# Kernel optimization log

Measured on AMD Instinct MI355X. Metric: run time of the kernel, lower is better.

## Reference

```python
import jax, jax.numpy as jnp
import numpy as np
import math

HIDDEN = 1024
HEADS = 16
HEAD = HIDDEN // HEADS
B, N = 2, 2048
NEG_INF = -10000.0


def setup_inputs() -> dict:
    key = jax.random.key(0)
    k1, k2, k3, k4, k5 = jax.random.split(key, 5)
    s = 1.0 / math.sqrt(HIDDEN)
    return {
        "encodings": jax.random.normal(k1, (B, N, HIDDEN), dtype=jnp.float32),
        "attn_w": jax.random.uniform(k2, (3 * HIDDEN, HIDDEN), minval=-s, maxval=s, dtype=jnp.float32),
        "attn_b": jax.random.uniform(k3, (3 * HIDDEN,), minval=-s, maxval=s, dtype=jnp.float32),
        "out_w": jax.random.uniform(k4, (HIDDEN, HIDDEN), minval=-s, maxval=s, dtype=jnp.float32),
        "out_b": jax.random.uniform(k5, (HIDDEN,), minval=-s, maxval=s, dtype=jnp.float32),
    }


def reference(encodings, attn_w, attn_b, out_w, out_b):
    b, n, _ = encodings.shape
    qkv = encodings @ attn_w.T + attn_b                      # [b, n, 3*hidden]
    # 'b n (h l) -> b h n l' with l = 3*head_size
    qkv = qkv.reshape(b, n, HEADS, 3 * HEAD).transpose(0, 2, 1, 3)  # [b, h, n, 3d]
    q, k, v = jnp.split(qkv, 3, axis=-1)                     # each [b, h, n, d]
    # causal mask: key index k attends only if k <= q
    mask = jnp.arange(n)[:, None] <= jnp.arange(n)[None, :]  # [k, q]
    scores = jnp.einsum('bhki,bhqi->bhkq', k, q) / math.sqrt(HEAD)
    scores = jnp.where(mask, scores, NEG_INF)
    probs = jax.nn.softmax(scores, axis=2)                   # softmax over k
    combined = jnp.einsum('bhkq,bhkl->bhql', probs, v)       # [b, h, n, d]
    out = combined.transpose(0, 2, 1, 3).reshape(b, n, HIDDEN)
    return out @ out_w.T + out_b
```

## Files before the change

kernel.cpp:

```cpp
#include <hip/hip_runtime.h>
#include <hip/hip_bf16.h>
#include <stdint.h>

#define HIDDEN 1024
#define NHEADS 16
#define DHEAD  64
#define BATCH  2
#define SEQ    2048
#define MROWS  (BATCH*SEQ)
#define QKVC   (3*HIDDEN)

typedef unsigned short u16;
typedef unsigned int   u32;
typedef __bf16 bf16x8 __attribute__((ext_vector_type(8)));
typedef __bf16 bf16x2 __attribute__((ext_vector_type(2)));
typedef float  f32x4  __attribute__((ext_vector_type(4)));
typedef float  f32x16 __attribute__((ext_vector_type(16)));
typedef short  s16x4  __attribute__((ext_vector_type(4)));
typedef u16    u16x8  __attribute__((ext_vector_type(8)));
typedef u32    u32x2  __attribute__((ext_vector_type(2)));

typedef const __attribute__((address_space(1))) void gvoid_t;
typedef       __attribute__((address_space(3))) void lvoid_t;

__device__ __forceinline__ gvoid_t* to_glob(const void* p){
  return (gvoid_t*)(uintptr_t)p;
}
__device__ __forceinline__ lvoid_t* to_lds(void* p){
  return (lvoid_t*)(uintptr_t)p;
}
__device__ __forceinline__ u32 lds_off(const void* p){
  return (u32)(uintptr_t)p;
}

__device__ __forceinline__ u16 f2bf(float x){
  __bf16 h = (__bf16)x;
  return __builtin_bit_cast(u16, h);
}
__device__ __forceinline__ u32 pk2(float a, float b){
  bf16x2 t = { (__bf16)a, (__bf16)b };
  return __builtin_bit_cast(u32, t);
}

#define MFMA32(a, b, c) __builtin_amdgcn_mfma_f32_32x32x16_bf16(a, b, c, 0, 0, 0)

#define CVT_N0 1048576
#define CVT_N1  786432
#define CVT_N2  262144
__global__ __launch_bounds__(256) void k_cvt3(const float* __restrict__ e,
                                              const float* __restrict__ wa,
                                              const float* __restrict__ wo,
                                              u16* __restrict__ eb,
                                              u16* __restrict__ wab,
                                              u16* __restrict__ wob){
  int i = blockIdx.x * 256 + threadIdx.x;
  const float* src; u16* dst;
  if (i < CVT_N0){ src = e; dst = eb; }
  else if (i < CVT_N0 + CVT_N1){ i -= CVT_N0; src = wa; dst = wab; }
  else if (i < CVT_N0 + CVT_N1 + CVT_N2){ i -= CVT_N0 + CVT_N1; src = wo; dst = wob; }
  else return;
  const float4 v = reinterpret_cast<const float4*>(src)[i];
  ushort4 o;
  o.x = f2bf(v.x); o.y = f2bf(v.y); o.z = f2bf(v.z); o.w = f2bf(v.w);
  reinterpret_cast<ushort4*>(dst)[i] = o;
}

template<int NC, bool BF16OUT>
__global__ __launch_bounds__(256) void k_gemm(const u16* __restrict__ A,
                                              const u16* __restrict__ B,
                                              const float* __restrict__ bias,
                                              void* __restrict__ C){
  constexpr int K = HIDDEN;
  __shared__ u16 As[2][128*32];
  __shared__ u16 Bs[2][128*32];
  const int lin = blockIdx.x + gridDim.x * blockIdx.y;
  const int xcd = lin & 7;
  const int pos = lin >> 3;
  const int mt  = pos & 31;
  const int nt  = xcd * (gridDim.y >> 3) + (pos >> 5);
  const int m0 = mt * 128;
  const int n0 = nt * 128;
  const int tid = threadIdx.x;
  const int w = tid >> 6, l = tid & 63;
  const int wr = w >> 1, wc = w & 1;

  const f32x4 fz = {0.f, 0.f, 0.f, 0.f};
  f32x4 acc[4][4];
  #pragma unroll
  for (int i = 0; i < 4; ++i)
    #pragma unroll
    for (int j = 0; j < 4; ++j) acc[i][j] = fz;

  const u16* ap = A + (size_t)(m0 + (tid >> 2)) * K + (tid & 3) * 8;
  const u16* bp = B + (size_t)(n0 + (tid >> 2)) * K + (tid & 3) * 8;

  auto stage = [&](int k0, int buf){
    __builtin_amdgcn_global_load_lds(to_glob(ap + k0),        to_lds(&As[buf][w*512]),        16, 0, 0);
    __builtin_amdgcn_global_load_lds(to_glob(ap + 64*K + k0), to_lds(&As[buf][2048 + w*512]), 16, 0, 0);
    __builtin_amdgcn_global_load_lds(to_glob(bp + k0),        to_lds(&Bs[buf][w*512]),        16, 0, 0);
    __builtin_amdgcn_global_load_lds(to_glob(bp + 64*K + k0), to_lds(&Bs[buf][2048 + w*512]), 16, 0, 0);
  };

  stage(0, 0);
  __syncthreads();

  for (int k0 = 0; k0 < K; k0 += 32){
    const int cur = (k0 >> 5) & 1;
    if (k0 + 32 < K) stage(k0 + 32, cur ^ 1);

    bf16x8 af[4], bfr[4];
    #pragma unroll
    for (int mf = 0; mf < 4; ++mf)
      af[mf]  = *(const bf16x8*)&As[cur][(wr*64 + mf*16 + (l & 15))*32 + (l >> 4)*8];
    #pragma unroll
    for (int nf = 0; nf < 4; ++nf)
      bfr[nf] = *(const bf16x8*)&Bs[cur][(wc*64 + nf*16 + (l & 15))*32 + (l >> 4)*8];
    #pragma unroll
    for (int mf = 0; mf < 4; ++mf)
      #pragma unroll
      for (int nf = 0; nf < 4; ++nf)
        acc[mf][nf] = __builtin_amdgcn_mfma_f32_16x16x32_bf16(af[mf], bfr[nf], acc[mf][nf], 0, 0, 0);

    __syncthreads();
  }

  #pragma unroll
  for (int nf = 0; nf < 4; ++nf){
    const int col = n0 + wc*64 + nf*16 + (l & 15);
    const float bv = bias[col];
    #pragma unroll
    for (int mf = 0; mf < 4; ++mf){
      #pragma unroll
      for (int r = 0; r < 4; ++r){
        const int row = m0 + wr*64 + mf*16 + (l >> 4)*4 + r;
        const float v = acc[mf][nf][r] + bv;
        if constexpr (BF16OUT) ((u16*)C)[(size_t)row * NC + col] = f2bf(v);
        else                   ((float*)C)[(size_t)row * NC + col] = v;
      }
    }
  }
}

__global__ __launch_bounds__(256, 4) void k_attn(const u16* __restrict__ qkv,
                                                 u16* __restrict__ aout){
  __shared__ u16 smem[20480];

  const int bh = blockIdx.x;
  const int b  = bh >> 4;
  const int h  = bh & 15;
  const int qt = 31 - blockIdx.y;
  const int tid = threadIdx.x;
  const int l  = tid & 63;
  const int w  = tid >> 6;
  const int hr = w >> 1;
  const int wr = w & 1;
  const int t128 = tid & 127;
  const int lw = t128 >> 6;
  const int U  = qt + 1;
  const int kb = hr ? U : 0;
  const int kmax = kb + U - 1;
  const int q0 = qt*64 + wr*32;
  const size_t base = (size_t)b * SEQ * QKVC + (size_t)h * 192;
  const float CEXP = 0.18033688011112042f;

  u16* const Kreg = smem + hr*10240;
  u16* const Vreg = smem + hr*10240 + 6144;

  const int cgK = (t128 & 7) ^ ((t128 >> 3) & 7);
  const u16* const baseK = qkv + base + (size_t)(t128 >> 3) * QKVC + 64 + cgK * 8;
  const int vk = ((t128 >> 5) << 2) | ((t128 >> 1) & 3);
  const int vd = (((t128 >> 3) & 3) << 4) | ((t128 & 1) << 3);
  const u16* const baseV = qkv + base + (size_t)vk * QKVC + 128 + vd;

  auto stageK = [&](int u, int cb){
    const u16* pk = baseK + (size_t)u * 32 * QKVC;
    #pragma unroll
    for (int t = 0; t < 2; ++t)
      __builtin_amdgcn_global_load_lds(to_glob(pk + t*16*QKVC),
                                       to_lds(&Kreg[cb*2048 + t*1024 + lw*512]), 16, 0, 0);
  };
  auto stageV = [&](int u, int vb){
    const u16* pv = baseV + (size_t)u * 32 * QKVC;
    #pragma unroll
    for (int t = 0; t < 2; ++t)
      __builtin_amdgcn_global_load_lds(to_glob(pv + t*16*QKVC),
                                       to_lds(&Vreg[vb*2048 + t*1024 + lw*512]), 16, 0, 0);
  };

  bf16x8 qf[4];
  {
    const u16* qp = qkv + base + (size_t)(q0 + (l & 31)) * QKVC + (l >> 5) * 8;
    #pragma unroll
    for (int dd = 0; dd < 4; ++dd) qf[dd] = *(const bf16x8*)(qp + dd*16);
  }

  f32x16 o0{}, o1{};
  float m = -1e30f, lsum = 0.f;

  stageK(kb, 0);
  stageV(kb, 0);
  stageK(kb + (U > 1 ? 1 : 0), 1);

  const u32 vbytes = lds_off(Vreg) + (l & 15)*8 + ((l >> 4) & 1)*128 + (l >> 5)*1024;

  int cb3 = 0;
  int vb2 = 0;
  for (int it = 0; it < U; ++it){
    const int u = kb + it;

    asm volatile("s_waitcnt vmcnt(2)" ::: "memory");
    __builtin_amdgcn_sched_barrier(0);
    __builtin_amdgcn_s_barrier();
    __builtin_amdgcn_sched_barrier(0);

    stageV(u + 1 > kmax ? kmax : u + 1, vb2 ^ 1);
    stageK(u + 2 > kmax ? kmax : u + 2, cb3 == 0 ? 2 : cb3 - 1);

    f32x16 a0{};
    const int r0 = l & 31;
    __builtin_amdgcn_s_setprio(1);
    #pragma unroll
    for (int dd = 0; dd < 4; ++dd){
      const int c = dd*2 + (l >> 5);
      const bf16x8 k0 = *(const bf16x8*)&Kreg[cb3*2048 + r0*64 + ((c ^ (r0 & 7)))*8];
      a0 = MFMA32(k0, qf[dd], a0);
    }
    __builtin_amdgcn_s_setprio(0);

    if (u*32 + 31 > q0){
      const int qg = q0 + (l & 31);
      #pragma unroll
      for (int r = 0; r < 16; ++r){
        const int kg = u*32 + (r & 3) + 8*(r >> 2) + 4*(l >> 5);
        if (kg > qg) a0[r] = -1e30f;
      }
    }

    float t8[8];
    #pragma unroll
    for (int r = 0; r < 8; ++r) t8[r] = fmaxf(a0[2*r], a0[2*r + 1]);
    #pragma unroll
    for (int s = 4; s > 0; s >>= 1)
      #pragma unroll
      for (int r = 0; r < s; ++r) t8[r] = fmaxf(t8[r], t8[r + s]);
    float pm = t8[0];
    pm = fmaxf(pm, __shfl(pm, l ^ 32));

    s16x4 tr[8];
    {
      const u32 vb = vbytes + (u32)vb2 * 4096u;
      #pragma unroll
      for (int kk = 0; kk < 2; ++kk){
        asm volatile("ds_read_b64_tr_b16 %0, %4 offset:0\n\t"
                     "ds_read_b64_tr_b16 %1, %4 offset:512\n\t"
                     "ds_read_b64_tr_b16 %2, %4 offset:256\n\t"
                     "ds_read_b64_tr_b16 %3, %4 offset:768"
                     : "=&v"(tr[kk*4+0]), "=&v"(tr[kk*4+1]),
                       "=&v"(tr[kk*4+2]), "=&v"(tr[kk*4+3])
                     : "v"(vb + kk*2048));
      }
    }

    if (__any(pm > m + 64.f)){
      const float mn = fmaxf(m, pm);
      const float corr = exp2f((m - mn) * CEXP);
      m = mn;
      lsum *= corr;
      #pragma unroll
      for (int r = 0; r < 16; ++r){
        const int row = (r & 3) + 8*(r >> 2) + 4*(l >> 5);
        const float cr = __shfl(corr, row | (l & 32));
        o0[r] *= cr; o1[r] *= cr;
      }
    }
    {
      float ls0 = 0.f, ls1 = 0.f;
      #pragma unroll
      for (int r = 0; r < 16; r += 2){
        const float p0 = exp2f((a0[r]   - m) * CEXP);
        const float p1 = exp2f((a0[r+1] - m) * CEXP);
        ls0 += p0; ls1 += p1;
        a0[r] = p0; a0[r+1] = p1;
      }
      lsum += ls0 + ls1;
    }

    asm volatile("s_waitcnt lgkmcnt(0)" ::: "memory");
    __builtin_amdgcn_sched_barrier(0);
    __builtin_amdgcn_s_setprio(1);
    #pragma unroll
    for (int kk = 0; kk < 2; ++kk){
      const int o = kk * 8;
      const u32 x0 = pk2(a0[o+0], a0[o+1]);
      const u32 x1 = pk2(a0[o+2], a0[o+3]);
      const u32 y0 = pk2(a0[o+4], a0[o+5]);
      const u32 y1 = pk2(a0[o+6], a0[o+7]);
      const u32x2 r0v = __builtin_amdgcn_permlane32_swap(x0, y0, false, false);
      const u32x2 r1v = __builtin_amdgcn_permlane32_swap(x1, y1, false, false);
      union { u32 wd[4]; bf16x8 v; } af;
      af.wd[0] = r0v[0]; af.wd[1] = r1v[0]; af.wd[2] = r0v[1]; af.wd[3] = r1v[1];
      union { s16x4 hh[2]; bf16x8 v; } b0, b1;
      b0.hh[0] = tr[kk*4+0]; b0.hh[1] = tr[kk*4+1];
      b1.hh[0] = tr[kk*4+2]; b1.hh[1] = tr[kk*4+3];
      o0 = MFMA32(af.v, b0.v, o0);
      o1 = MFMA32(af.v, b1.v, o1);
    }
    __builtin_amdgcn_s_setprio(0);

    cb3 = (cb3 == 2) ? 0 : cb3 + 1;
    vb2 ^= 1;
  }

  lsum += __shfl(lsum, l ^ 32);
  __syncthreads();
  float* const Osh  = (float*)smem;
  float2* const MLsh = (float2*)((char*)smem + 16384);

  if (hr == 1){
    #pragma unroll
    for (int r = 0; r < 16; ++r){
      Osh[wr*2048 + l*32 + r]      = o0[r];
      Osh[wr*2048 + l*32 + 16 + r] = o1[r];
    }
    MLsh[wr*64 + l] = float2{m, lsum};
  }
  __syncthreads();

  if (hr == 0){
    const float2 ml1 = MLsh[wr*64 + l];
    const float mm = fmaxf(m, ml1.x);
    const float c0 = exp2f((m - mm) * CEXP);
    const float c1 = exp2f((ml1.x - mm) * CEXP);
    const float lm = lsum*c0 + ml1.y*c1;
    const float a0q = c0 / lm;
    const float a1q = c1 / lm;
    #pragma unroll
    for (int r = 0; r < 16; ++r){
      const int row = (r & 3) + 8*(r >> 2) + 4*(l >> 5);
      const float f0 = __shfl(a0q, row | (l & 32));
      const float f1 = __shfl(a1q, row | (l & 32));
      const int qg = q0 + row;
      u16* op = aout + (size_t)(b*SEQ + qg) * HIDDEN + h*64 + (l & 31);
      op[0]  = f2bf(o0[r]*f0 + Osh[wr*2048 + l*32 + r]*f1);
      op[32] = f2bf(o1[r]*f0 + Osh[wr*2048 + l*32 + 16 + r]*f1);
    }
  }
}

extern "C" void kernel_launch(void* const* d_in, const int* in_sizes, int n_in,
                              void* d_out, int out_size, void* d_ws, size_t ws_size,
                              hipStream_t stream){
  const float* enc    = (const float*)d_in[0];
  const float* attn_w = (const float*)d_in[1];
  const float* attn_b = (const float*)d_in[2];
  const float* out_w  = (const float*)d_in[3];
  const float* out_b  = (const float*)d_in[4];

  char* ws = (char*)d_ws;
  u16* enc_bf = (u16*)(ws);
  u16* wa_bf  = (u16*)(ws + (size_t)( 8u << 20));
  u16* wo_bf  = (u16*)(ws + (size_t)(14u << 20));
  u16* qkv    = (u16*)(ws + (size_t)(16u << 20));
  u16* aout   = enc_bf;

  k_cvt3<<<dim3((CVT_N0+CVT_N1+CVT_N2 + 255)/256), 256, 0, stream>>>(
      enc, attn_w, out_w, enc_bf, wa_bf, wo_bf);

  k_gemm<QKVC,  true ><<<dim3(MROWS/128, QKVC/128),  256, 0, stream>>>(enc_bf, wa_bf, attn_b, qkv);
  k_attn<<<dim3(32, 32), 256, 0, stream>>>(qkv, aout);
  k_gemm<HIDDEN, false><<<dim3(MROWS/128, HIDDEN/128), 256, 0, stream>>>(aout, wo_bf, out_b, d_out);
}
```

Measured before the change: 108.3 us.

## Pair light and heavy causal query tiles per block for balanced attention work

The attention kernel now launches 512-thread blocks that each handle two query tiles (p and 31-p), so every block does the same 17 iterations of causal KV work instead of work that varies with the tile index. Four KV split domains per block share the total, and a multi-stage LDS merge combines the partial softmax states. This is meant to remove tail imbalance from causal masking and halve the grid. In exchange it doubles LDS use per block, adds extra barriers and merge passes, and drops the setprio hints.

```diff
diff --git a/kernel.cpp b/kernel.cpp
--- a/kernel.cpp
+++ b/kernel.cpp
@@ -141,35 +141,35 @@
   }
 }
 
-__global__ __launch_bounds__(256, 4) void k_attn(const u16* __restrict__ qkv,
+__global__ __launch_bounds__(512, 4) void k_attn(const u16* __restrict__ qkv,
                                                  u16* __restrict__ aout){
-  __shared__ u16 smem[20480];
+  __shared__ u16 smem[40960];
 
   const int bh = blockIdx.x;
   const int b  = bh >> 4;
   const int h  = bh & 15;
-  const int qt = 31 - blockIdx.y;
+  const int p  = blockIdx.y;
+  const int gA = p, gB = 31 - p;
   const int tid = threadIdx.x;
   const int l  = tid & 63;
   const int w  = tid >> 6;
-  const int hr = w >> 1;
-  const int wr = w & 1;
-  const int t128 = tid & 127;
-  const int lw = t128 >> 6;
-  const int U  = qt + 1;
-  const int kb = hr ? U : 0;
-  const int kmax = kb + U - 1;
-  const int q0 = qt*64 + wr*32;
+  const int hr = w & 1;
+  const int wr = (w >> 1) & 1;
+  const int gp = w >> 2;
+  const int dom = gp*2 + hr;
+  const int dlane = wr*64 + l;
+  const int UA = p + 1, UB = 32 - p;
+  const int kbA = hr * UA, kbB = hr * UB;
   const size_t base = (size_t)b * SEQ * QKVC + (size_t)h * 192;
   const float CEXP = 0.18033688011112042f;
 
-  u16* const Kreg = smem + hr*10240;
-  u16* const Vreg = smem + hr*10240 + 6144;
-
-  const int cgK = (t128 & 7) ^ ((t128 >> 3) & 7);
-  const u16* const baseK = qkv + base + (size_t)(t128 >> 3) * QKVC + 64 + cgK * 8;
-  const int vk = ((t128 >> 5) << 2) | ((t128 >> 1) & 3);
-  const int vd = (((t128 >> 3) & 3) << 4) | ((t128 & 1) << 3);
+  u16* const Kreg = smem + dom*10240;
+  u16* const Vreg = smem + dom*10240 + 6144;
+
+  const int cgK = (dlane & 7) ^ ((dlane >> 3) & 7);
+  const u16* const baseK = qkv + base + (size_t)(dlane >> 3) * QKVC + 64 + cgK * 8;
+  const int vk = ((dlane >> 5) << 2) | ((dlane >> 1) & 3);
+  const int vd = (((dlane >> 3) & 3) << 4) | ((dlane & 1) << 3);
   const u16* const baseV = qkv + base + (size_t)vk * QKVC + 128 + vd;
 
   auto stageK = [&](int u, int cb){
@@ -177,135 +177,154 @@
     #pragma unroll
     for (int t = 0; t < 2; ++t)
       __builtin_amdgcn_global_load_lds(to_glob(pk + t*16*QKVC),
-                                       to_lds(&Kreg[cb*2048 + t*1024 + lw*512]), 16, 0, 0);
+                                       to_lds(&Kreg[cb*2048 + t*1024 + wr*512]), 16, 0, 0);
   };
   auto stageV = [&](int u, int vb){
     const u16* pv = baseV + (size_t)u * 32 * QKVC;
     #pragma unroll
     for (int t = 0; t < 2; ++t)
       __builtin_amdgcn_global_load_lds(to_glob(pv + t*16*QKVC),
-                                       to_lds(&Vreg[vb*2048 + t*1024 + lw*512]), 16, 0, 0);
-  };
-
+                                       to_lds(&Vreg[vb*2048 + t*1024 + wr*512]), 16, 0, 0);
+  };
+
+  auto unit_of = [&](int t)->int{
+    if (t > 16) t = 16;
+    if (gp) return kbB + t;
+    if (t <= p) return kbA + t;
+    int uu = kbB + 17 + (t - p - 1);
+    const int um = kbB + UB - 1;
+    return uu > um ? um : uu;
+  };
+
+  int q0s = (gp ? gB : gA)*64 + wr*32;
   bf16x8 qf[4];
   {
-    const u16* qp = qkv + base + (size_t)(q0 + (l & 31)) * QKVC + (l >> 5) * 8;
+    const u16* qp = qkv + base + (size_t)(q0s + (l & 31)) * QKVC + (l >> 5) * 8;
     #pragma unroll
     for (int dd = 0; dd < 4; ++dd) qf[dd] = *(const bf16x8*)(qp + dd*16);
   }
 
   f32x16 o0{}, o1{};
   float m = -1e30f, lsum = 0.f;
-
-  stageK(kb, 0);
-  stageV(kb, 0);
-  stageK(kb + (U > 1 ? 1 : 0), 1);
+  f32x16 so0{}, so1{};
+  float sm = -1e30f, sl = 0.f;
+
+  stageK(unit_of(0), 0);
+  stageV(unit_of(0), 0);
+  stageK(unit_of(1), 1);
 
   const u32 vbytes = lds_off(Vreg) + (l & 15)*8 + ((l >> 4) & 1)*128 + (l >> 5)*1024;
 
-  int cb3 = 0;
-  int vb2 = 0;
-  for (int it = 0; it < U; ++it){
-    const int u = kb + it;
-
+  int cb3 = 0, vb2 = 0;
+  for (int t = 0; t < 17; ++t){
     asm volatile("s_waitcnt vmcnt(2)" ::: "memory");
     __builtin_amdgcn_sched_barrier(0);
     __builtin_amdgcn_s_barrier();
     __builtin_amdgcn_sched_barrier(0);
 
-    stageV(u + 1 > kmax ? kmax : u + 1, vb2 ^ 1);
-    stageK(u + 2 > kmax ? kmax : u + 2, cb3 == 0 ? 2 : cb3 - 1);
-
-    f32x16 a0{};
-    const int r0 = l & 31;
-    __builtin_amdgcn_s_setprio(1);
-    #pragma unroll
-    for (int dd = 0; dd < 4; ++dd){
-      const int c = dd*2 + (l >> 5);
-      const bf16x8 k0 = *(const bf16x8*)&Kreg[cb3*2048 + r0*64 + ((c ^ (r0 & 7)))*8];
-      a0 = MFMA32(k0, qf[dd], a0);
-    }
-    __builtin_amdgcn_s_setprio(0);
-
-    if (u*32 + 31 > q0){
-      const int qg = q0 + (l & 31);
-      #pragma unroll
-      for (int r = 0; r < 16; ++r){
-        const int kg = u*32 + (r & 3) + 8*(r >> 2) + 4*(l >> 5);
-        if (kg > qg) a0[r] = -1e30f;
-      }
-    }
-
-    float t8[8];
-    #pragma unroll
-    for (int r = 0; r < 8; ++r) t8[r] = fmaxf(a0[2*r], a0[2*r + 1]);
-    #pragma unroll
-    for (int s = 4; s > 0; s >>= 1)
-      #pragma unroll
-      for (int r = 0; r < s; ++r) t8[r] = fmaxf(t8[r], t8[r + s]);
-    float pm = t8[0];
-    pm = fmaxf(pm, __shfl(pm, l ^ 32));
-
-    s16x4 tr[8];
-    {
-      const u32 vb = vbytes + (u32)vb2 * 4096u;
+    stageV(unit_of(t + 1), vb2 ^ 1);
+    stageK(unit_of(t + 2), cb3 == 0 ? 2 : cb3 - 1);
+
+    if (gp == 0 && t == p + 1){
+      lsum += __shfl(lsum, l ^ 32);
+      sm = m; sl = lsum; so0 = o0; so1 = o1;
+      m = -1e30f; lsum = 0.f;
+      #pragma unroll
+      for (int r = 0; r < 16; ++r){ o0[r] = 0.f; o1[r] = 0.f; }
+      q0s = gB*64 + wr*32;
+      const u16* qp = qkv + base + (size_t)(q0s + (l & 31)) * QKVC + (l >> 5) * 8;
+      #pragma unroll
+      for (int dd = 0; dd < 4; ++dd) qf[dd] = *(const bf16x8*)(qp + dd*16);
+      asm volatile("s_waitcnt vmcnt(0)" ::: "memory");
+      __builtin_amdgcn_sched_barrier(0);
+    }
+
+    const bool act = gp ? true : (t < 16);
+    if (act){
+      const int u = unit_of(t);
+
+      f32x16 a0{};
+      const int r0 = l & 31;
+      #pragma unroll
+      for (int dd = 0; dd < 4; ++dd){
+        const int c = dd*2 + (l >> 5);
+        const bf16x8 k0 = *(const bf16x8*)&Kreg[cb3*2048 + r0*64 + ((c ^ (r0 & 7)))*8];
+        a0 = MFMA32(k0, qf[dd], a0);
+      }
+
+      if (u*32 + 31 > q0s){
+        const int qg = q0s + (l & 31);
+        #pragma unroll
+        for (int r = 0; r < 16; ++r){
+          const int kg = u*32 + (r & 3) + 8*(r >> 2) + 4*(l >> 5);
+          if (kg > qg) a0[r] = -1e30f;
+        }
+      }
+
+      float pm = -1e30f;
+      #pragma unroll
+      for (int r = 0; r < 16; ++r) pm = fmaxf(pm, a0[r]);
+      pm = fmaxf(pm, __shfl(pm, l ^ 32));
+
+      s16x4 tr[8];
+      {
+        const u32 vb = vbytes + (u32)vb2 * 4096u;
+        #pragma unroll
+        for (int kk = 0; kk < 2; ++kk){
+          asm volatile("ds_read_b64_tr_b16 %0, %4 offset:0\n\t"
+                       "ds_read_b64_tr_b16 %1, %4 offset:512\n\t"
+                       "ds_read_b64_tr_b16 %2, %4 offset:256\n\t"
+                       "ds_read_b64_tr_b16 %3, %4 offset:768"
+                       : "=&v"(tr[kk*4+0]), "=&v"(tr[kk*4+1]),
+                         "=&v"(tr[kk*4+2]), "=&v"(tr[kk*4+3])
+                       : "v"(vb + kk*2048));
+        }
+      }
+
+      if (__any(pm > m + 64.f)){
+        const float mn = fmaxf(m, pm);
+        const float corr = exp2f((m - mn) * CEXP);
+        m = mn;
+        lsum *= corr;
+        #pragma unroll
+        for (int r = 0; r < 16; ++r){
+          const int row = (r & 3) + 8*(r >> 2) + 4*(l >> 5);
+          const float cr = __shfl(corr, row | (l & 32));
+          o0[r] *= cr; o1[r] *= cr;
+        }
+      }
+      {
+        float ls0 = 0.f, ls1 = 0.f;
+        #pragma unroll
+        for (int r = 0; r < 16; r += 2){
+          const float p0 = exp2f((a0[r]   - m) * CEXP);
+          const float p1 = exp2f((a0[r+1] - m) * CEXP);
+          ls0 += p0; ls1 += p1;
+          a0[r] = p0; a0[r+1] = p1;
+        }
+        lsum += ls0 + ls1;
+      }
+
+      asm volatile("s_waitcnt lgkmcnt(0)" ::: "memory");
+      __builtin_amdgcn_sched_barrier(0);
       #pragma unroll
       for (int kk = 0; kk < 2; ++kk){
-        asm volatile("ds_read_b64_tr_b16 %0, %4 offset:0\n\t"
-                     "ds_read_b64_tr_b16 %1, %4 offset:512\n\t"
-                     "ds_read_b64_tr_b16 %2, %4 offset:256\n\t"
-                     "ds_read_b64_tr_b16 %3, %4 offset:768"
-                     : "=&v"(tr[kk*4+0]), "=&v"(tr[kk*4+1]),
-                       "=&v"(tr[kk*4+2]), "=&v"(tr[kk*4+3])
-                     : "v"(vb + kk*2048));
-      }
-    }
-
-    if (__any(pm > m + 64.f)){
-      const float mn = fmaxf(m, pm);
-      const float corr = exp2f((m - mn) * CEXP);
-      m = mn;
-      lsum *= corr;
-      #pragma unroll
-      for (int r = 0; r < 16; ++r){
-        const int row = (r & 3) + 8*(r >> 2) + 4*(l >> 5);
-        const float cr = __shfl(corr, row | (l & 32));
-        o0[r] *= cr; o1[r] *= cr;
-      }
-    }
-    {
-      float ls0 = 0.f, ls1 = 0.f;
-      #pragma unroll
-      for (int r = 0; r < 16; r += 2){
-        const float p0 = exp2f((a0[r]   - m) * CEXP);
-        const float p1 = exp2f((a0[r+1] - m) * CEXP);
-        ls0 += p0; ls1 += p1;
-        a0[r] = p0; a0[r+1] = p1;
-      }
-      lsum += ls0 + ls1;
-    }
-
-    asm volatile("s_waitcnt lgkmcnt(0)" ::: "memory");
-    __builtin_amdgcn_sched_barrier(0);
-    __builtin_amdgcn_s_setprio(1);
-    #pragma unroll
-    for (int kk = 0; kk < 2; ++kk){
-      const int o = kk * 8;
-      const u32 x0 = pk2(a0[o+0], a0[o+1]);
-      const u32 x1 = pk2(a0[o+2], a0[o+3]);
-      const u32 y0 = pk2(a0[o+4], a0[o+5]);
-      const u32 y1 = pk2(a0[o+6], a0[o+7]);
-      const u32x2 r0v = __builtin_amdgcn_permlane32_swap(x0, y0, false, false);
-      const u32x2 r1v = __builtin_amdgcn_permlane32_swap(x1, y1, false, false);
-      union { u32 wd[4]; bf16x8 v; } af;
-      af.wd[0] = r0v[0]; af.wd[1] = r1v[0]; af.wd[2] = r0v[1]; af.wd[3] = r1v[1];
-      union { s16x4 hh[2]; bf16x8 v; } b0, b1;
-      b0.hh[0] = tr[kk*4+0]; b0.hh[1] = tr[kk*4+1];
-      b1.hh[0] = tr[kk*4+2]; b1.hh[1] = tr[kk*4+3];
-      o0 = MFMA32(af.v, b0.v, o0);
-      o1 = MFMA32(af.v, b1.v, o1);
-    }
-    __builtin_amdgcn_s_setprio(0);
+        const int o = kk * 8;
+        const u32 x0 = pk2(a0[o+0], a0[o+1]);
+        const u32 x1 = pk2(a0[o+2], a0[o+3]);
+        const u32 y0 = pk2(a0[o+4], a0[o+5]);
+        const u32 y1 = pk2(a0[o+6], a0[o+7]);
+        const u32x2 r0v = __builtin_amdgcn_permlane32_swap(x0, y0, false, false);
+        const u32x2 r1v = __builtin_amdgcn_permlane32_swap(x1, y1, false, false);
+        union { u32 wd[4]; bf16x8 v; } af;
+        af.wd[0] = r0v[0]; af.wd[1] = r1v[0]; af.wd[2] = r0v[1]; af.wd[3] = r1v[1];
+        union { s16x4 hh[2]; bf16x8 v; } b0v, b1v;
+        b0v.hh[0] = tr[kk*4+0]; b0v.hh[1] = tr[kk*4+1];
+        b1v.hh[0] = tr[kk*4+2]; b1v.hh[1] = tr[kk*4+3];
+        o0 = MFMA32(af.v, b0v.v, o0);
+        o1 = MFMA32(af.v, b1v.v, o1);
+      }
+    }
 
     cb3 = (cb3 == 2) ? 0 : cb3 + 1;
     vb2 ^= 1;
@@ -313,37 +332,69 @@
 
   lsum += __shfl(lsum, l ^ 32);
   __syncthreads();
-  float* const Osh  = (float*)smem;
-  float2* const MLsh = (float2*)((char*)smem + 16384);
-
-  if (hr == 1){
+
+  float*  const MOf  = (float*)smem;
+  float2* const MLml = (float2*)((char*)smem + 49152);
+
+  auto publish = [&](int s, float mm, float ll, const f32x16& p0, const f32x16& p1){
+    const int ws = s*2 + wr;
     #pragma unroll
     for (int r = 0; r < 16; ++r){
-      Osh[wr*2048 + l*32 + r]      = o0[r];
-      Osh[wr*2048 + l*32 + 16 + r] = o1[r];
-    }
-    MLsh[wr*64 + l] = float2{m, lsum};
-  }
-  __syncthreads();
-
-  if (hr == 0){
-    const float2 ml1 = MLsh[wr*64 + l];
-    const float mm = fmaxf(m, ml1.x);
-    const float c0 = exp2f((m - mm) * CEXP);
-    const float c1 = exp2f((ml1.x - mm) * CEXP);
-    const float lm = lsum*c0 + ml1.y*c1;
-    const float a0q = c0 / lm;
-    const float a1q = c1 / lm;
+      MOf[ws*2048 + l*32 + r]      = p0[r];
+      MOf[ws*2048 + l*32 + 16 + r] = p1[r];
+    }
+    MLml[s*128 + wr*64 + l] = float2{mm, ll};
+  };
+  auto mergeWith = [&](int s, float& mm, float& ll, f32x16& p0, f32x16& p1){
+    const int ws = s*2 + wr;
+    const float2 o2 = MLml[s*128 + wr*64 + l];
+    const float mx = fmaxf(mm, o2.x);
+    const float c1 = exp2f((mm   - mx) * CEXP);
+    const float c2 = exp2f((o2.x - mx) * CEXP);
     #pragma unroll
     for (int r = 0; r < 16; ++r){
       const int row = (r & 3) + 8*(r >> 2) + 4*(l >> 5);
-      const float f0 = __shfl(a0q, row | (l & 32));
-      const float f1 = __shfl(a1q, row | (l & 32));
-      const int qg = q0 + row;
+      const float cr1 = __shfl(c1, row | (l & 32));
+      const float cr2 = __shfl(c2, row | (l & 32));
+      p0[r] = p0[r]*cr1 + MOf[ws*2048 + l*32 + r]*cr2;
+      p1[r] = p1[r]*cr1 + MOf[ws*2048 + l*32 + 16 + r]*cr2;
+    }
+    mm = mx;
+    ll = ll*c1 + o2.y*c2;
+  };
+  auto writeOut = [&](int g, float ll, const f32x16& p0, const f32x16& p1){
+    const float inv = 1.0f / ll;
+    #pragma unroll
+    for (int r = 0; r < 16; ++r){
+      const int row = (r & 3) + 8*(r >> 2) + 4*(l >> 5);
+      const float ivr = __shfl(inv, row | (l & 32));
+      const int qg = g*64 + wr*32 + row;
       u16* op = aout + (size_t)(b*SEQ + qg) * HIDDEN + h*64 + (l & 31);
-      op[0]  = f2bf(o0[r]*f0 + Osh[wr*2048 + l*32 + r]*f1);
-      op[32] = f2bf(o1[r]*f0 + Osh[wr*2048 + l*32 + 16 + r]*f1);
-    }
+      op[0]  = f2bf(p0[r] * ivr);
+      op[32] = f2bf(p1[r] * ivr);
+    }
+  };
+
+  if (gp == 1 && hr == 1) publish(0, m, lsum, o0, o1);
+  if (gp == 0 && hr == 1){
+    publish(1, m, lsum, o0, o1);
+    publish(2, sm, sl, so0, so1);
+  }
+  __syncthreads();
+
+  if (gp == 1 && hr == 0) mergeWith(0, m, lsum, o0, o1);
+  if (gp == 0 && hr == 0){
+    mergeWith(2, sm, sl, so0, so1);
+    writeOut(gA, sl, so0, so1);
+    mergeWith(1, m, lsum, o0, o1);
+  }
+  __syncthreads();
+
+  if (gp == 0 && hr == 0) publish(0, m, lsum, o0, o1);
+  __syncthreads();
+  if (gp == 1 && hr == 0){
+    mergeWith(0, m, lsum, o0, o1);
+    writeOut(gB, lsum, o0, o1);
   }
 }
 
@@ -367,6 +418,6 @@
       enc, attn_w, out_w, enc_bf, wa_bf, wo_bf);
 
   k_gemm<QKVC,  true ><<<dim3(MROWS/128, QKVC/128),  256, 0, stream>>>(enc_bf, wa_bf, attn_b, qkv);
-  k_attn<<<dim3(32, 32), 256, 0, stream>>>(qkv, aout);
+  k_attn<<<dim3(32, 16), 512, 0, stream>>>(qkv, aout);
   k_gemm<HIDDEN, false><<<dim3(MROWS/128, HIDDEN/128), 256, 0, stream>>>(aout, wo_bf, out_b, d_out);
 }
```

Measured after the change: 130.8 us. 20.8% more time.
